# Kernel tuning notes

Hardware: AMD Instinct MI355X
Metric: run time of the kernel (lower is better)

## Reference

```python
import jax, jax.numpy as jnp
import numpy as np

N = 100000      # nodes
E = 3200000     # edges (avg degree 32)
F_IN = 128      # num_node_features
H = 16          # hidden dim (fixed in module)
C = 2           # num_classes


def setup_inputs() -> dict:
    key = jax.random.key(0)
    k0, k1, k2, k3 = jax.random.split(key, 4)
    x = jax.random.normal(k0, (N, F_IN), dtype=jnp.float32)
    edge_index = jax.random.randint(k1, (2, E), 0, N, dtype=jnp.int32)
    # GCNConv params: weight (in,out) + bias (out,) per layer (glorot-ish scale)
    W1 = jax.random.normal(k2, (F_IN, H), dtype=jnp.float32) * (1.0 / np.sqrt(F_IN))
    b1 = jnp.zeros((H,), jnp.float32)
    W2 = jax.random.normal(k3, (H, C), dtype=jnp.float32) * (1.0 / np.sqrt(H))
    b2 = jnp.zeros((C,), jnp.float32)
    return {"x": x, "edge_index": edge_index, "W1": W1, "b1": b1, "W2": W2, "b2": b2}


def _gcn_conv(x, W, b, src, dst, n):
    # GCNConv: h = D^{-1/2}(A+I)D^{-1/2} (x W) + b, with self-loops in src/dst
    h = x @ W                                   # [n, out]
    deg = jax.ops.segment_sum(jnp.ones_like(dst, dtype=h.dtype), dst, num_segments=n)
    dinv = jnp.where(deg > 0, jax.lax.rsqrt(deg), 0.0)
    norm = dinv[src] * dinv[dst]                # [E+n]
    msg = h[src] * norm[:, None]                # gather + scale
    out = jax.ops.segment_sum(msg, dst, num_segments=n)  # scatter-add
    return out + b


def reference(x, edge_index, W1, b1, W2, b2):
    loops = jnp.arange(N, dtype=edge_index.dtype)
    src = jnp.concatenate([edge_index[0], loops])
    dst = jnp.concatenate([edge_index[1], loops])
    h = jax.nn.relu(_gcn_conv(x, W1, b1, src, dst, N))
    # F.dropout(training=False) in eval mode is identity
    out = _gcn_conv(h, W2, b2, src, dst, N)
    return jax.nn.log_softmax(out, axis=1)
```

## Files before the change

### kernel.cpp

```cpp
#include <hip/hip_runtime.h>
#include <hip/hip_bf16.h>

#define NN 100000
#define NE 3200000
#define FIN 128
#define HD 16
#define CD 2

#define BSH 8
#define BSPAN 256
#define NBKT 391
#define CAP 9216
#define NPB 391

#define FXS 1048576.0f
#define FXI (1.0f / 1048576.0f)

__device__ __forceinline__ float lo2f(unsigned int u) {
    union { float f; unsigned int i; } v; v.i = u << 16; return v.f;
}
__device__ __forceinline__ float hi2f(unsigned int u) {
    union { float f; unsigned int i; } v; v.i = u & 0xFFFF0000u; return v.f;
}
__device__ __forceinline__ ushort f2b(float f) {
    union { float f; unsigned int u; } v; v.f = f;
    unsigned int r = (v.u + 0x7FFFu + ((v.u >> 16) & 1u)) >> 16;
    return (ushort)r;
}
__device__ __forceinline__ unsigned pck(float a, float b) {
    return (unsigned)f2b(a) | ((unsigned)f2b(b) << 16);
}

__global__ __launch_bounds__(512) void k_scat(const int* __restrict__ src,
                                              const int* __restrict__ dst,
                                              int* __restrict__ gcnt,
                                              unsigned int* __restrict__ csrb) {
    __shared__ int h[NBKT];
    __shared__ int cur[NBKT];
    int t = threadIdx.x;
    for (int i = t; i < NBKT; i += 512) h[i] = 0;
    __syncthreads();
    int cq = blockIdx.x * 2048;
    const int4* s4p = (const int4*)src;
    const int4* d4p = (const int4*)dst;
    int4 sv[4], dv[4];
    #pragma unroll
    for (int j = 0; j < 4; ++j) {
        int e4 = cq + j * 512 + t;
        if (e4 < NE / 4) {
            sv[j] = s4p[e4];
            dv[j] = d4p[e4];
            atomicAdd(&h[dv[j].x >> BSH], 1);
            atomicAdd(&h[dv[j].y >> BSH], 1);
            atomicAdd(&h[dv[j].z >> BSH], 1);
            atomicAdd(&h[dv[j].w >> BSH], 1);
        }
    }
    __syncthreads();
    for (int i = t; i < NBKT; i += 512) {
        int c = h[i];
        int base = c ? atomicAdd(&gcnt[i], c) : 0;
        cur[i] = i * CAP + base;
    }
    __syncthreads();
    #pragma unroll
    for (int j = 0; j < 4; ++j) {
        int e4 = cq + j * 512 + t;
        if (e4 < NE / 4) {
            int p;
            p = atomicAdd(&cur[dv[j].x >> BSH], 1);
            csrb[p] = (unsigned)sv[j].x | ((unsigned)(dv[j].x & (BSPAN - 1)) << 17);
            p = atomicAdd(&cur[dv[j].y >> BSH], 1);
            csrb[p] = (unsigned)sv[j].y | ((unsigned)(dv[j].y & (BSPAN - 1)) << 17);
            p = atomicAdd(&cur[dv[j].z >> BSH], 1);
            csrb[p] = (unsigned)sv[j].z | ((unsigned)(dv[j].z & (BSPAN - 1)) << 17);
            p = atomicAdd(&cur[dv[j].w >> BSH], 1);
            csrb[p] = (unsigned)sv[j].w | ((unsigned)(dv[j].w & (BSPAN - 1)) << 17);
        }
    }
}

__global__ __launch_bounds__(512) void k_gemm1d(const int* __restrict__ gcnt,
                                                const unsigned int* __restrict__ csrb,
                                                const float* __restrict__ x,
                                                const float* __restrict__ W1,
                                                float* __restrict__ dinv,
                                                ushort* __restrict__ h1b) {
    __shared__ float wsm[FIN][HD];
    __shared__ int cnt[BSPAN];
    __shared__ float dvs[BSPAN];
    int b = blockIdx.x, t = threadIdx.x;
    if (t < BSPAN) cnt[t] = 0;
    for (int i = t; i < FIN * HD; i += 512) wsm[i >> 4][i & 15] = W1[i];
    __syncthreads();
    int e0 = b * CAP, e1 = e0 + gcnt[b];
    for (int e = e0 + t; e < e1; e += 512) atomicAdd(&cnt[csrb[e] >> 17], 1);
    __syncthreads();
    if (t < BSPAN) {
        int node = b * BSPAN + t;
        float di = rsqrtf((float)cnt[t] + 1.0f);
        dvs[t] = di;
        if (node < NN) dinv[node] = di;
    }
    __syncthreads();
    int loc = t >> 1, half = t & 1;
    int node = b * BSPAN + loc;
    if (node >= NN) return;
    int g = half * 8;
    const float4* xr = (const float4*)(x + (size_t)node * FIN);
    float a0 = 0.f, a1 = 0.f, a2 = 0.f, a3 = 0.f;
    float a4 = 0.f, a5 = 0.f, a6 = 0.f, a7 = 0.f;
    #pragma unroll
    for (int k4 = 0; k4 < FIN / 4; ++k4) {
        float4 v = xr[k4];
        #pragma unroll
        for (int kk = 0; kk < 4; ++kk) {
            float vk = (kk == 0) ? v.x : (kk == 1) ? v.y : (kk == 2) ? v.z : v.w;
            float4 w0 = *(const float4*)&wsm[k4 * 4 + kk][g];
            float4 w1 = *(const float4*)&wsm[k4 * 4 + kk][g + 4];
            a0 += vk * w0.x; a1 += vk * w0.y; a2 += vk * w0.z; a3 += vk * w0.w;
            a4 += vk * w1.x; a5 += vk * w1.y; a6 += vk * w1.z; a7 += vk * w1.w;
        }
    }
    float di = dvs[loc];
    uint4 r = {pck(a0 * di, a1 * di), pck(a2 * di, a3 * di),
               pck(a4 * di, a5 * di), pck(a6 * di, a7 * di)};
    *(uint4*)(h1b + (size_t)node * HD + g) = r;
}

__device__ __forceinline__ void scat16(int* a, uint4 u0, uint4 u1) {
    atomicAdd(a + 0,  __float2int_rn(lo2f(u0.x) * FXS));
    atomicAdd(a + 1,  __float2int_rn(hi2f(u0.x) * FXS));
    atomicAdd(a + 2,  __float2int_rn(lo2f(u0.y) * FXS));
    atomicAdd(a + 3,  __float2int_rn(hi2f(u0.y) * FXS));
    atomicAdd(a + 4,  __float2int_rn(lo2f(u0.z) * FXS));
    atomicAdd(a + 5,  __float2int_rn(hi2f(u0.z) * FXS));
    atomicAdd(a + 6,  __float2int_rn(lo2f(u0.w) * FXS));
    atomicAdd(a + 7,  __float2int_rn(hi2f(u0.w) * FXS));
    atomicAdd(a + 8,  __float2int_rn(lo2f(u1.x) * FXS));
    atomicAdd(a + 9,  __float2int_rn(hi2f(u1.x) * FXS));
    atomicAdd(a + 10, __float2int_rn(lo2f(u1.y) * FXS));
    atomicAdd(a + 11, __float2int_rn(hi2f(u1.y) * FXS));
    atomicAdd(a + 12, __float2int_rn(lo2f(u1.z) * FXS));
    atomicAdd(a + 13, __float2int_rn(hi2f(u1.z) * FXS));
    atomicAdd(a + 14, __float2int_rn(lo2f(u1.w) * FXS));
    atomicAdd(a + 15, __float2int_rn(hi2f(u1.w) * FXS));
}

__global__ __launch_bounds__(512) void k_aggs1(const int* __restrict__ gcnt,
                                               const unsigned int* __restrict__ csrb,
                                               const ushort* __restrict__ h1b,
                                               const float* __restrict__ dinv,
                                               const float* __restrict__ b1,
                                               const float* __restrict__ W2,
                                               float* __restrict__ g_s) {
    __shared__ int acc[BSPAN][HD + 1];
    __shared__ float w2s[HD * 2];
    __shared__ float b1s[HD];
    int b = blockIdx.x, t = threadIdx.x;
    for (int i = t; i < BSPAN * (HD + 1); i += 512) ((int*)acc)[i] = 0;
    if (t < HD * 2) w2s[t] = W2[t];
    else if (t < HD * 3) b1s[t - HD * 2] = b1[t - HD * 2];
    __syncthreads();
    int e0 = b * CAP, e1 = e0 + gcnt[b];
    int e = e0 + t;
    for (; e + 512 < e1; e += 1024) {
        unsigned pa = csrb[e];
        unsigned pb = csrb[e + 512];
        const uint4* ra = (const uint4*)(h1b + (size_t)(pa & 0x1FFFF) * HD);
        const uint4* rb = (const uint4*)(h1b + (size_t)(pb & 0x1FFFF) * HD);
        uint4 a0 = ra[0], a1 = ra[1];
        uint4 c0 = rb[0], c1 = rb[1];
        scat16(acc[pa >> 17], a0, a1);
        scat16(acc[pb >> 17], c0, c1);
    }
    if (e < e1) {
        unsigned p = csrb[e];
        const uint4* r = (const uint4*)(h1b + (size_t)(p & 0x1FFFF) * HD);
        uint4 u0 = r[0], u1 = r[1];
        scat16(acc[p >> 17], u0, u1);
    }
    __syncthreads();
    int loc = t >> 1, half = t & 1;
    int node = b * BSPAN + loc;
    if (node < NN) {
        float di = dinv[node];
        const uint4 sv = *(const uint4*)(h1b + (size_t)node * HD + half * 8);
        float sf[8] = {lo2f(sv.x), hi2f(sv.x), lo2f(sv.y), hi2f(sv.y),
                       lo2f(sv.z), hi2f(sv.z), lo2f(sv.w), hi2f(sv.w)};
        const int* a = acc[loc] + half * 8;
        const float* bb = b1s + half * 8;
        const float* ww = w2s + half * 16;
        float p0 = 0.f, p1 = 0.f;
        #pragma unroll
        for (int k = 0; k < 8; ++k) {
            float v = fmaxf(di * ((float)a[k] * FXI + sf[k]) + bb[k], 0.f);
            p0 += v * ww[k * 2];
            p1 += v * ww[k * 2 + 1];
        }
        p0 += __shfl_xor(p0, 1, 64);
        p1 += __shfl_xor(p1, 1, 64);
        if (half == 0) {
            float2 r = {p0 * di, p1 * di};
            *(float2*)(g_s + (size_t)node * 2) = r;
        }
    }
}

__global__ __launch_bounds__(512) void k_aggs2(const int* __restrict__ gcnt,
                                               const unsigned int* __restrict__ csrb,
                                               const float* __restrict__ g_s,
                                               const float* __restrict__ dinv,
                                               const float* __restrict__ b2,
                                               float* __restrict__ out) {
    __shared__ int acc[BSPAN * 3];
    int b = blockIdx.x, t = threadIdx.x;
    for (int i = t; i < BSPAN * 3; i += 512) acc[i] = 0;
    __syncthreads();
    int e0 = b * CAP, e1 = e0 + gcnt[b];
    int e = e0 + t;
    for (; e + 512 < e1; e += 1024) {
        unsigned pa = csrb[e];
        unsigned pb = csrb[e + 512];
        float2 va = *(const float2*)(g_s + (size_t)(pa & 0x1FFFF) * 2);
        float2 vb = *(const float2*)(g_s + (size_t)(pb & 0x1FFFF) * 2);
        int la = (pa >> 17) * 3, lb = (pb >> 17) * 3;
        atomicAdd(&acc[la],     __float2int_rn(va.x * FXS));
        atomicAdd(&acc[la + 1], __float2int_rn(va.y * FXS));
        atomicAdd(&acc[lb],     __float2int_rn(vb.x * FXS));
        atomicAdd(&acc[lb + 1], __float2int_rn(vb.y * FXS));
    }
    if (e < e1) {
        unsigned p = csrb[e];
        float2 v = *(const float2*)(g_s + (size_t)(p & 0x1FFFF) * 2);
        int l = (p >> 17) * 3;
        atomicAdd(&acc[l],     __float2int_rn(v.x * FXS));
        atomicAdd(&acc[l + 1], __float2int_rn(v.y * FXS));
    }
    __syncthreads();
    if (t < BSPAN) {
        int node = b * BSPAN + t;
        if (node < NN) {
            float di = dinv[node];
            float2 sv = *(const float2*)(g_s + (size_t)node * 2);
            float o0 = di * ((float)acc[t * 3] * FXI + sv.x) + b2[0];
            float o1 = di * ((float)acc[t * 3 + 1] * FXI + sv.y) + b2[1];
            float mx = fmaxf(o0, o1);
            float l = mx + logf(__expf(o0 - mx) + __expf(o1 - mx));
            float2 r = {o0 - l, o1 - l};
            *(float2*)(out + (size_t)node * 2) = r;
        }
    }
}

extern "C" void kernel_launch(void* const* d_in, const int* in_sizes, int n_in,
                              void* d_out, int out_size, void* d_ws, size_t ws_size,
                              hipStream_t stream) {
    const float* x   = (const float*)d_in[0];
    const int* ei    = (const int*)d_in[1];
    const int* src   = ei;
    const int* dst   = ei + NE;
    const float* W1  = (const float*)d_in[2];
    const float* b1  = (const float*)d_in[3];
    const float* W2  = (const float*)d_in[4];
    const float* b2  = (const float*)d_in[5];
    float* out = (float*)d_out;

    char* w = (char*)d_ws;
    int*   gcnt        = (int*)w;            w += NBKT * 4;
    float* dinv        = (float*)w;          w += NN * 4;
    unsigned int* csrb = (unsigned int*)w;   w += (size_t)NBKT * CAP * 4;
    ushort* h1b        = (ushort*)w;         w += (size_t)NN * HD * 2;
    float* g_s         = (float*)w;          w += NN * CD * 4;

    hipMemsetAsync(gcnt, 0, NBKT * 4, stream);
    k_scat   <<<NPB, 512, 0, stream>>>(src, dst, gcnt, csrb);
    k_gemm1d <<<NBKT, 512, 0, stream>>>(gcnt, csrb, x, W1, dinv, h1b);
    k_aggs1  <<<NBKT, 512, 0, stream>>>(gcnt, csrb, h1b, dinv, b1, W2, g_s);
    k_aggs2  <<<NBKT, 512, 0, stream>>>(gcnt, csrb, g_s, dinv, b2, out);
}
```

Before: 200.6 us.

## Fuse all GCN stages into one persistent kernel with grid barriers

Merges the four kernels into a single persistent kernel of 391 blocks that synchronise through a software grid barrier built on global atomics, and keeps the per-node degree scaling in shared memory instead of a global dinv array. The bucket scatter now stages edges in LDS, prefix-sums the bucket counts, and writes contiguous runs to the global CSR buffer, which should make those writes better coalesced. This removes three launch boundaries, but it depends on every block being co-resident for the spin barrier to avoid deadlock, and the larger union of shared memory may lower occupancy.

```diff
diff --git a/kernel.cpp b/kernel.cpp
--- a/kernel.cpp
+++ b/kernel.cpp
@@ -1,131 +1,60 @@
 #include <hip/hip_runtime.h>
-#include <hip/hip_bf16.h>
 
 #define NN 100000
 #define NE 3200000
 #define FIN 128
 #define HD 16
-#define CD 2
 
 #define BSH 8
 #define BSPAN 256
 #define NBKT 391
 #define CAP 9216
-#define NPB 391
+#define TPB 512
 
 #define FXS 1048576.0f
 #define FXI (1.0f / 1048576.0f)
 
-__device__ __forceinline__ float lo2f(unsigned int u) {
-    union { float f; unsigned int i; } v; v.i = u << 16; return v.f;
-}
-__device__ __forceinline__ float hi2f(unsigned int u) {
-    union { float f; unsigned int i; } v; v.i = u & 0xFFFF0000u; return v.f;
+__device__ __forceinline__ float lo2f(unsigned u) {
+    union { float f; unsigned i; } v; v.i = u << 16; return v.f;
+}
+__device__ __forceinline__ float hi2f(unsigned u) {
+    union { float f; unsigned i; } v; v.i = u & 0xFFFF0000u; return v.f;
 }
 __device__ __forceinline__ ushort f2b(float f) {
-    union { float f; unsigned int u; } v; v.f = f;
-    unsigned int r = (v.u + 0x7FFFu + ((v.u >> 16) & 1u)) >> 16;
+    union { float f; unsigned u; } v; v.f = f;
+    unsigned r = (v.u + 0x7FFFu + ((v.u >> 16) & 1u)) >> 16;
     return (ushort)r;
 }
 __device__ __forceinline__ unsigned pck(float a, float b) {
     return (unsigned)f2b(a) | ((unsigned)f2b(b) << 16);
 }
 
-__global__ __launch_bounds__(512) void k_scat(const int* __restrict__ src,
-                                              const int* __restrict__ dst,
-                                              int* __restrict__ gcnt,
-                                              unsigned int* __restrict__ csrb) {
-    __shared__ int h[NBKT];
-    __shared__ int cur[NBKT];
-    int t = threadIdx.x;
-    for (int i = t; i < NBKT; i += 512) h[i] = 0;
-    __syncthreads();
-    int cq = blockIdx.x * 2048;
-    const int4* s4p = (const int4*)src;
-    const int4* d4p = (const int4*)dst;
-    int4 sv[4], dv[4];
-    #pragma unroll
-    for (int j = 0; j < 4; ++j) {
-        int e4 = cq + j * 512 + t;
-        if (e4 < NE / 4) {
-            sv[j] = s4p[e4];
-            dv[j] = d4p[e4];
-            atomicAdd(&h[dv[j].x >> BSH], 1);
-            atomicAdd(&h[dv[j].y >> BSH], 1);
-            atomicAdd(&h[dv[j].z >> BSH], 1);
-            atomicAdd(&h[dv[j].w >> BSH], 1);
-        }
-    }
-    __syncthreads();
-    for (int i = t; i < NBKT; i += 512) {
-        int c = h[i];
-        int base = c ? atomicAdd(&gcnt[i], c) : 0;
-        cur[i] = i * CAP + base;
-    }
-    __syncthreads();
-    #pragma unroll
-    for (int j = 0; j < 4; ++j) {
-        int e4 = cq + j * 512 + t;
-        if (e4 < NE / 4) {
-            int p;
-            p = atomicAdd(&cur[dv[j].x >> BSH], 1);
-            csrb[p] = (unsigned)sv[j].x | ((unsigned)(dv[j].x & (BSPAN - 1)) << 17);
-            p = atomicAdd(&cur[dv[j].y >> BSH], 1);
-            csrb[p] = (unsigned)sv[j].y | ((unsigned)(dv[j].y & (BSPAN - 1)) << 17);
-            p = atomicAdd(&cur[dv[j].z >> BSH], 1);
-            csrb[p] = (unsigned)sv[j].z | ((unsigned)(dv[j].z & (BSPAN - 1)) << 17);
-            p = atomicAdd(&cur[dv[j].w >> BSH], 1);
-            csrb[p] = (unsigned)sv[j].w | ((unsigned)(dv[j].w & (BSPAN - 1)) << 17);
-        }
-    }
-}
-
-__global__ __launch_bounds__(512) void k_gemm1d(const int* __restrict__ gcnt,
-                                                const unsigned int* __restrict__ csrb,
-                                                const float* __restrict__ x,
-                                                const float* __restrict__ W1,
-                                                float* __restrict__ dinv,
-                                                ushort* __restrict__ h1b) {
-    __shared__ float wsm[FIN][HD];
-    __shared__ int cnt[BSPAN];
-    __shared__ float dvs[BSPAN];
-    int b = blockIdx.x, t = threadIdx.x;
-    if (t < BSPAN) cnt[t] = 0;
-    for (int i = t; i < FIN * HD; i += 512) wsm[i >> 4][i & 15] = W1[i];
-    __syncthreads();
-    int e0 = b * CAP, e1 = e0 + gcnt[b];
-    for (int e = e0 + t; e < e1; e += 512) atomicAdd(&cnt[csrb[e] >> 17], 1);
-    __syncthreads();
-    if (t < BSPAN) {
-        int node = b * BSPAN + t;
-        float di = rsqrtf((float)cnt[t] + 1.0f);
-        dvs[t] = di;
-        if (node < NN) dinv[node] = di;
-    }
-    __syncthreads();
-    int loc = t >> 1, half = t & 1;
-    int node = b * BSPAN + loc;
-    if (node >= NN) return;
-    int g = half * 8;
-    const float4* xr = (const float4*)(x + (size_t)node * FIN);
-    float a0 = 0.f, a1 = 0.f, a2 = 0.f, a3 = 0.f;
-    float a4 = 0.f, a5 = 0.f, a6 = 0.f, a7 = 0.f;
-    #pragma unroll
-    for (int k4 = 0; k4 < FIN / 4; ++k4) {
-        float4 v = xr[k4];
-        #pragma unroll
-        for (int kk = 0; kk < 4; ++kk) {
-            float vk = (kk == 0) ? v.x : (kk == 1) ? v.y : (kk == 2) ? v.z : v.w;
-            float4 w0 = *(const float4*)&wsm[k4 * 4 + kk][g];
-            float4 w1 = *(const float4*)&wsm[k4 * 4 + kk][g + 4];
-            a0 += vk * w0.x; a1 += vk * w0.y; a2 += vk * w0.z; a3 += vk * w0.w;
-            a4 += vk * w1.x; a5 += vk * w1.y; a6 += vk * w1.z; a7 += vk * w1.w;
-        }
-    }
-    float di = dvs[loc];
-    uint4 r = {pck(a0 * di, a1 * di), pck(a2 * di, a3 * di),
-               pck(a4 * di, a5 * di), pck(a6 * di, a7 * di)};
-    *(uint4*)(h1b + (size_t)node * HD + g) = r;
+union SMem {
+    struct { int h[NBKT]; int sbuf[TPB]; int lcur[NBKT]; int gbase[NBKT];
+             unsigned ebuf[8192]; } s;
+    struct { float wsm[FIN][HD]; int cnt[BSPAN]; } g;
+    struct { int acc[BSPAN][HD + 1]; float w2s[HD * 2]; float b1s[HD]; } a1;
+    struct { int acc2[BSPAN * 3]; } a2;
+};
+
+__device__ __forceinline__ void gbar(int* bar, int phase) {
+    __syncthreads();
+    if (threadIdx.x == 0) {
+        __threadfence();
+        __hip_atomic_fetch_add(&bar[0], 1, __ATOMIC_RELEASE, __HIP_MEMORY_SCOPE_AGENT);
+        if (blockIdx.x == 0) {
+            while (__hip_atomic_load(&bar[0], __ATOMIC_ACQUIRE, __HIP_MEMORY_SCOPE_AGENT)
+                   < phase * NBKT)
+                __builtin_amdgcn_s_sleep(4);
+            __hip_atomic_store(&bar[1], phase, __ATOMIC_RELEASE, __HIP_MEMORY_SCOPE_AGENT);
+        } else {
+            while (__hip_atomic_load(&bar[1], __ATOMIC_ACQUIRE, __HIP_MEMORY_SCOPE_AGENT)
+                   < phase)
+                __builtin_amdgcn_s_sleep(4);
+        }
+        __threadfence();
+    }
+    __syncthreads();
 }
 
 __device__ __forceinline__ void scat16(int* a, uint4 u0, uint4 u1) {
@@ -147,104 +76,200 @@
     atomicAdd(a + 15, __float2int_rn(hi2f(u1.w) * FXS));
 }
 
-__global__ __launch_bounds__(512) void k_aggs1(const int* __restrict__ gcnt,
-                                               const unsigned int* __restrict__ csrb,
-                                               const ushort* __restrict__ h1b,
-                                               const float* __restrict__ dinv,
-                                               const float* __restrict__ b1,
-                                               const float* __restrict__ W2,
-                                               float* __restrict__ g_s) {
-    __shared__ int acc[BSPAN][HD + 1];
-    __shared__ float w2s[HD * 2];
-    __shared__ float b1s[HD];
+__global__ __launch_bounds__(TPB, 4) void k_all(
+    const int* __restrict__ src, const int* __restrict__ dst,
+    const float* __restrict__ x, const float* __restrict__ W1,
+    const float* __restrict__ b1, const float* __restrict__ W2,
+    const float* __restrict__ b2,
+    int* __restrict__ gcnt, int* __restrict__ bar,
+    unsigned* __restrict__ csrb, ushort* __restrict__ h1b,
+    float* __restrict__ g_s, float* __restrict__ out)
+{
+    __shared__ SMem sm;
+    __shared__ float dvs[BSPAN];
     int b = blockIdx.x, t = threadIdx.x;
-    for (int i = t; i < BSPAN * (HD + 1); i += 512) ((int*)acc)[i] = 0;
-    if (t < HD * 2) w2s[t] = W2[t];
-    else if (t < HD * 3) b1s[t - HD * 2] = b1[t - HD * 2];
-    __syncthreads();
+
+    for (int i = t; i < NBKT; i += TPB) sm.s.h[i] = 0;
+    __syncthreads();
+    int cq = b * 2048;
+    const int4* s4p = (const int4*)src;
+    const int4* d4p = (const int4*)dst;
+    int4 sv[4], dv[4];
+    #pragma unroll
+    for (int j = 0; j < 4; ++j) {
+        int e4 = cq + j * TPB + t;
+        if (e4 < NE / 4) {
+            sv[j] = s4p[e4]; dv[j] = d4p[e4];
+            atomicAdd(&sm.s.h[dv[j].x >> BSH], 1);
+            atomicAdd(&sm.s.h[dv[j].y >> BSH], 1);
+            atomicAdd(&sm.s.h[dv[j].z >> BSH], 1);
+            atomicAdd(&sm.s.h[dv[j].w >> BSH], 1);
+        }
+    }
+    __syncthreads();
+    sm.s.sbuf[t] = (t < NBKT) ? sm.s.h[t] : 0;
+    __syncthreads();
+    for (int off = 1; off < TPB; off <<= 1) {
+        int v = 0;
+        if (t >= off) v = sm.s.sbuf[t - off];
+        __syncthreads();
+        if (t >= off) sm.s.sbuf[t] += v;
+        __syncthreads();
+    }
+    if (t < NBKT) {
+        int c = sm.s.h[t];
+        int excl = sm.s.sbuf[t] - c;
+        sm.s.lcur[t] = excl;
+        int gb = t * CAP - excl;
+        if (c) gb += atomicAdd(&gcnt[t], c);
+        sm.s.gbase[t] = gb;
+    }
+    __syncthreads();
+    #pragma unroll
+    for (int j = 0; j < 4; ++j) {
+        int e4 = cq + j * TPB + t;
+        if (e4 < NE / 4) {
+            int bk, p;
+            bk = dv[j].x >> BSH; p = atomicAdd(&sm.s.lcur[bk], 1);
+            sm.s.ebuf[p] = (unsigned)sv[j].x | ((unsigned)(dv[j].x & (BSPAN - 1)) << 17);
+            bk = dv[j].y >> BSH; p = atomicAdd(&sm.s.lcur[bk], 1);
+            sm.s.ebuf[p] = (unsigned)sv[j].y | ((unsigned)(dv[j].y & (BSPAN - 1)) << 17);
+            bk = dv[j].z >> BSH; p = atomicAdd(&sm.s.lcur[bk], 1);
+            sm.s.ebuf[p] = (unsigned)sv[j].z | ((unsigned)(dv[j].z & (BSPAN - 1)) << 17);
+            bk = dv[j].w >> BSH; p = atomicAdd(&sm.s.lcur[bk], 1);
+            sm.s.ebuf[p] = (unsigned)sv[j].w | ((unsigned)(dv[j].w & (BSPAN - 1)) << 17);
+        }
+    }
+    __syncthreads();
+    int ecnt = NE - b * 8192; if (ecnt > 8192) ecnt = 8192;
+    for (int p = t; p < ecnt; p += TPB) {
+        unsigned pl = sm.s.ebuf[p];
+        int lo = 0, hi = NBKT;
+        while (lo < hi) { int mid = (lo + hi) >> 1;
+                          if (sm.s.sbuf[mid] > p) hi = mid; else lo = mid + 1; }
+        csrb[sm.s.gbase[lo] + p] = pl;
+    }
+    gbar(bar, 1);
+
     int e0 = b * CAP, e1 = e0 + gcnt[b];
-    int e = e0 + t;
-    for (; e + 512 < e1; e += 1024) {
-        unsigned pa = csrb[e];
-        unsigned pb = csrb[e + 512];
-        const uint4* ra = (const uint4*)(h1b + (size_t)(pa & 0x1FFFF) * HD);
-        const uint4* rb = (const uint4*)(h1b + (size_t)(pb & 0x1FFFF) * HD);
-        uint4 a0 = ra[0], a1 = ra[1];
-        uint4 c0 = rb[0], c1 = rb[1];
-        scat16(acc[pa >> 17], a0, a1);
-        scat16(acc[pb >> 17], c0, c1);
-    }
-    if (e < e1) {
-        unsigned p = csrb[e];
-        const uint4* r = (const uint4*)(h1b + (size_t)(p & 0x1FFFF) * HD);
-        uint4 u0 = r[0], u1 = r[1];
-        scat16(acc[p >> 17], u0, u1);
-    }
-    __syncthreads();
-    int loc = t >> 1, half = t & 1;
-    int node = b * BSPAN + loc;
-    if (node < NN) {
-        float di = dinv[node];
-        const uint4 sv = *(const uint4*)(h1b + (size_t)node * HD + half * 8);
-        float sf[8] = {lo2f(sv.x), hi2f(sv.x), lo2f(sv.y), hi2f(sv.y),
-                       lo2f(sv.z), hi2f(sv.z), lo2f(sv.w), hi2f(sv.w)};
-        const int* a = acc[loc] + half * 8;
-        const float* bb = b1s + half * 8;
-        const float* ww = w2s + half * 16;
-        float p0 = 0.f, p1 = 0.f;
-        #pragma unroll
-        for (int k = 0; k < 8; ++k) {
-            float v = fmaxf(di * ((float)a[k] * FXI + sf[k]) + bb[k], 0.f);
-            p0 += v * ww[k * 2];
-            p1 += v * ww[k * 2 + 1];
-        }
-        p0 += __shfl_xor(p0, 1, 64);
-        p1 += __shfl_xor(p1, 1, 64);
-        if (half == 0) {
-            float2 r = {p0 * di, p1 * di};
-            *(float2*)(g_s + (size_t)node * 2) = r;
-        }
-    }
-}
-
-__global__ __launch_bounds__(512) void k_aggs2(const int* __restrict__ gcnt,
-                                               const unsigned int* __restrict__ csrb,
-                                               const float* __restrict__ g_s,
-                                               const float* __restrict__ dinv,
-                                               const float* __restrict__ b2,
-                                               float* __restrict__ out) {
-    __shared__ int acc[BSPAN * 3];
-    int b = blockIdx.x, t = threadIdx.x;
-    for (int i = t; i < BSPAN * 3; i += 512) acc[i] = 0;
-    __syncthreads();
-    int e0 = b * CAP, e1 = e0 + gcnt[b];
-    int e = e0 + t;
-    for (; e + 512 < e1; e += 1024) {
-        unsigned pa = csrb[e];
-        unsigned pb = csrb[e + 512];
-        float2 va = *(const float2*)(g_s + (size_t)(pa & 0x1FFFF) * 2);
-        float2 vb = *(const float2*)(g_s + (size_t)(pb & 0x1FFFF) * 2);
-        int la = (pa >> 17) * 3, lb = (pb >> 17) * 3;
-        atomicAdd(&acc[la],     __float2int_rn(va.x * FXS));
-        atomicAdd(&acc[la + 1], __float2int_rn(va.y * FXS));
-        atomicAdd(&acc[lb],     __float2int_rn(vb.x * FXS));
-        atomicAdd(&acc[lb + 1], __float2int_rn(vb.y * FXS));
-    }
-    if (e < e1) {
-        unsigned p = csrb[e];
-        float2 v = *(const float2*)(g_s + (size_t)(p & 0x1FFFF) * 2);
-        int l = (p >> 17) * 3;
-        atomicAdd(&acc[l],     __float2int_rn(v.x * FXS));
-        atomicAdd(&acc[l + 1], __float2int_rn(v.y * FXS));
+    for (int i = t; i < FIN * HD; i += TPB) sm.g.wsm[i >> 4][i & 15] = W1[i];
+    if (t < BSPAN) sm.g.cnt[t] = 0;
+    __syncthreads();
+    for (int e = e0 + t; e < e1; e += TPB) atomicAdd(&sm.g.cnt[csrb[e] >> 17], 1);
+    __syncthreads();
+    if (t < BSPAN) dvs[t] = rsqrtf((float)sm.g.cnt[t] + 1.0f);
+    __syncthreads();
+    {
+        int loc = t >> 1, half = t & 1;
+        int node = b * BSPAN + loc;
+        if (node < NN) {
+            int g8 = half * 8;
+            const float4* xr = (const float4*)(x + (size_t)node * FIN);
+            float a0 = 0.f, a1 = 0.f, a2 = 0.f, a3 = 0.f;
+            float a4 = 0.f, a5 = 0.f, a6 = 0.f, a7 = 0.f;
+            #pragma unroll
+            for (int k4 = 0; k4 < FIN / 4; ++k4) {
+                float4 v = xr[k4];
+                #pragma unroll
+                for (int kk = 0; kk < 4; ++kk) {
+                    float vk = (kk == 0) ? v.x : (kk == 1) ? v.y : (kk == 2) ? v.z : v.w;
+                    float4 w0 = *(const float4*)&sm.g.wsm[k4 * 4 + kk][g8];
+                    float4 w1 = *(const float4*)&sm.g.wsm[k4 * 4 + kk][g8 + 4];
+                    a0 += vk * w0.x; a1 += vk * w0.y; a2 += vk * w0.z; a3 += vk * w0.w;
+                    a4 += vk * w1.x; a5 += vk * w1.y; a6 += vk * w1.z; a7 += vk * w1.w;
+                }
+            }
+            float di = dvs[loc];
+            uint4 r = {pck(a0 * di, a1 * di), pck(a2 * di, a3 * di),
+                       pck(a4 * di, a5 * di), pck(a6 * di, a7 * di)};
+            *(uint4*)(h1b + (size_t)node * HD + g8) = r;
+        }
+    }
+    gbar(bar, 2);
+
+    for (int i = t; i < BSPAN * (HD + 1); i += TPB) ((int*)sm.a1.acc)[i] = 0;
+    if (t < HD * 2) sm.a1.w2s[t] = W2[t];
+    else if (t < HD * 3) sm.a1.b1s[t - HD * 2] = b1[t - HD * 2];
+    __syncthreads();
+    {
+        int e = e0 + t;
+        for (; e + TPB < e1; e += 2 * TPB) {
+            unsigned pa = csrb[e];
+            unsigned pb = csrb[e + TPB];
+            const uint4* ra = (const uint4*)(h1b + (size_t)(pa & 0x1FFFF) * HD);
+            const uint4* rb = (const uint4*)(h1b + (size_t)(pb & 0x1FFFF) * HD);
+            uint4 a0 = ra[0], a1 = ra[1];
+            uint4 c0 = rb[0], c1 = rb[1];
+            scat16(sm.a1.acc[pa >> 17], a0, a1);
+            scat16(sm.a1.acc[pb >> 17], c0, c1);
+        }
+        if (e < e1) {
+            unsigned p = csrb[e];
+            const uint4* r = (const uint4*)(h1b + (size_t)(p & 0x1FFFF) * HD);
+            uint4 u0 = r[0], u1 = r[1];
+            scat16(sm.a1.acc[p >> 17], u0, u1);
+        }
+    }
+    __syncthreads();
+    {
+        int loc = t >> 1, half = t & 1;
+        int node = b * BSPAN + loc;
+        if (node < NN) {
+            float di = dvs[loc];
+            const uint4 svv = *(const uint4*)(h1b + (size_t)node * HD + half * 8);
+            float sf[8] = {lo2f(svv.x), hi2f(svv.x), lo2f(svv.y), hi2f(svv.y),
+                           lo2f(svv.z), hi2f(svv.z), lo2f(svv.w), hi2f(svv.w)};
+            const int* a = sm.a1.acc[loc] + half * 8;
+            const float* bb = sm.a1.b1s + half * 8;
+            const float* ww = sm.a1.w2s + half * 16;
+            float p0 = 0.f, p1 = 0.f;
+            #pragma unroll
+            for (int k = 0; k < 8; ++k) {
+                float v = fmaxf(di * ((float)a[k] * FXI + sf[k]) + bb[k], 0.f);
+                p0 += v * ww[k * 2];
+                p1 += v * ww[k * 2 + 1];
+            }
+            p0 += __shfl_xor(p0, 1, 64);
+            p1 += __shfl_xor(p1, 1, 64);
+            if (half == 0) {
+                float2 r = {p0 * di, p1 * di};
+                *(float2*)(g_s + (size_t)node * 2) = r;
+            }
+        }
+    }
+    gbar(bar, 3);
+
+    for (int i = t; i < BSPAN * 3; i += TPB) sm.a2.acc2[i] = 0;
+    __syncthreads();
+    {
+        int e = e0 + t;
+        for (; e + TPB < e1; e += 2 * TPB) {
+            unsigned pa = csrb[e];
+            unsigned pb = csrb[e + TPB];
+            float2 va = *(const float2*)(g_s + (size_t)(pa & 0x1FFFF) * 2);
+            float2 vb = *(const float2*)(g_s + (size_t)(pb & 0x1FFFF) * 2);
+            int la = (pa >> 17) * 3, lb = (pb >> 17) * 3;
+            atomicAdd(&sm.a2.acc2[la],     __float2int_rn(va.x * FXS));
+            atomicAdd(&sm.a2.acc2[la + 1], __float2int_rn(va.y * FXS));
+            atomicAdd(&sm.a2.acc2[lb],     __float2int_rn(vb.x * FXS));
+            atomicAdd(&sm.a2.acc2[lb + 1], __float2int_rn(vb.y * FXS));
+        }
+        if (e < e1) {
+            unsigned p = csrb[e];
+            float2 v = *(const float2*)(g_s + (size_t)(p & 0x1FFFF) * 2);
+            int l = (p >> 17) * 3;
+            atomicAdd(&sm.a2.acc2[l],     __float2int_rn(v.x * FXS));
+            atomicAdd(&sm.a2.acc2[l + 1], __float2int_rn(v.y * FXS));
+        }
     }
     __syncthreads();
     if (t < BSPAN) {
         int node = b * BSPAN + t;
         if (node < NN) {
-            float di = dinv[node];
-            float2 sv = *(const float2*)(g_s + (size_t)node * 2);
-            float o0 = di * ((float)acc[t * 3] * FXI + sv.x) + b2[0];
-            float o1 = di * ((float)acc[t * 3 + 1] * FXI + sv.y) + b2[1];
+            float di = dvs[t];
+            float2 svv = *(const float2*)(g_s + (size_t)node * 2);
+            float o0 = di * ((float)sm.a2.acc2[t * 3] * FXI + svv.x) + b2[0];
+            float o1 = di * ((float)sm.a2.acc2[t * 3 + 1] * FXI + svv.y) + b2[1];
             float mx = fmaxf(o0, o1);
             float l = mx + logf(__expf(o0 - mx) + __expf(o1 - mx));
             float2 r = {o0 - l, o1 - l};
@@ -268,14 +293,12 @@
 
     char* w = (char*)d_ws;
     int*   gcnt        = (int*)w;            w += NBKT * 4;
-    float* dinv        = (float*)w;          w += NN * 4;
+    int*   bar         = (int*)w;            w += 2 * 4;
     unsigned int* csrb = (unsigned int*)w;   w += (size_t)NBKT * CAP * 4;
     ushort* h1b        = (ushort*)w;         w += (size_t)NN * HD * 2;
-    float* g_s         = (float*)w;          w += NN * CD * 4;
-
-    hipMemsetAsync(gcnt, 0, NBKT * 4, stream);
-    k_scat   <<<NPB, 512, 0, stream>>>(src, dst, gcnt, csrb);
-    k_gemm1d <<<NBKT, 512, 0, stream>>>(gcnt, csrb, x, W1, dinv, h1b);
-    k_aggs1  <<<NBKT, 512, 0, stream>>>(gcnt, csrb, h1b, dinv, b1, W2, g_s);
-    k_aggs2  <<<NBKT, 512, 0, stream>>>(gcnt, csrb, g_s, dinv, b2, out);
-}
+    float* g_s         = (float*)w;          w += NN * 2 * 4;
+
+    hipMemsetAsync(gcnt, 0, (NBKT + 2) * 4, stream);
+    k_all<<<NBKT, TPB, 0, stream>>>(src, dst, x, W1, b1, W2, b2,
+                                    gcnt, bar, csrb, h1b, g_s, out);
+}
```

Measured after the change: 504.5 us. +151.5%, slower.

## Stage edge scatter in shared memory sorted by bucket before global writes

Applied to the files above, without the earlier changes.

The bucketing kernel now computes a block-local prefix sum over bucket counts and places each edge into a shared-memory buffer ordered by bucket. It then writes the buffer to global memory in linear order, finding each entry's bucket by binary search, so consecutive threads write contiguous runs instead of scattering single words. This is meant to cut uncoalesced global stores in the CSR build. The cost is about 32KB of extra shared memory per block, which may lower occupancy, plus a scan and a per-element binary search.

```diff
diff --git a/kernel.cpp b/kernel.cpp
--- a/kernel.cpp
+++ b/kernel.cpp
@@ -1,55 +1,55 @@
 #include <hip/hip_runtime.h>
-#include <hip/hip_bf16.h>
 
 #define NN 100000
 #define NE 3200000
 #define FIN 128
 #define HD 16
-#define CD 2
 
 #define BSH 8
 #define BSPAN 256
 #define NBKT 391
 #define CAP 9216
-#define NPB 391
+#define TPB 512
 
 #define FXS 1048576.0f
 #define FXI (1.0f / 1048576.0f)
 
-__device__ __forceinline__ float lo2f(unsigned int u) {
-    union { float f; unsigned int i; } v; v.i = u << 16; return v.f;
-}
-__device__ __forceinline__ float hi2f(unsigned int u) {
-    union { float f; unsigned int i; } v; v.i = u & 0xFFFF0000u; return v.f;
+__device__ __forceinline__ float lo2f(unsigned u) {
+    union { float f; unsigned i; } v; v.i = u << 16; return v.f;
+}
+__device__ __forceinline__ float hi2f(unsigned u) {
+    union { float f; unsigned i; } v; v.i = u & 0xFFFF0000u; return v.f;
 }
 __device__ __forceinline__ ushort f2b(float f) {
-    union { float f; unsigned int u; } v; v.f = f;
-    unsigned int r = (v.u + 0x7FFFu + ((v.u >> 16) & 1u)) >> 16;
+    union { float f; unsigned u; } v; v.f = f;
+    unsigned r = (v.u + 0x7FFFu + ((v.u >> 16) & 1u)) >> 16;
     return (ushort)r;
 }
 __device__ __forceinline__ unsigned pck(float a, float b) {
     return (unsigned)f2b(a) | ((unsigned)f2b(b) << 16);
 }
 
-__global__ __launch_bounds__(512) void k_scat(const int* __restrict__ src,
+__global__ __launch_bounds__(TPB) void k_scat(const int* __restrict__ src,
                                               const int* __restrict__ dst,
                                               int* __restrict__ gcnt,
-                                              unsigned int* __restrict__ csrb) {
+                                              unsigned* __restrict__ csrb) {
     __shared__ int h[NBKT];
-    __shared__ int cur[NBKT];
-    int t = threadIdx.x;
-    for (int i = t; i < NBKT; i += 512) h[i] = 0;
-    __syncthreads();
-    int cq = blockIdx.x * 2048;
+    __shared__ int sbuf[TPB];
+    __shared__ int lcur[NBKT];
+    __shared__ int gbase[NBKT];
+    __shared__ unsigned ebuf[8192];
+    int b = blockIdx.x, t = threadIdx.x;
+    for (int i = t; i < NBKT; i += TPB) h[i] = 0;
+    __syncthreads();
+    int cq = b * 2048;
     const int4* s4p = (const int4*)src;
     const int4* d4p = (const int4*)dst;
     int4 sv[4], dv[4];
     #pragma unroll
     for (int j = 0; j < 4; ++j) {
-        int e4 = cq + j * 512 + t;
+        int e4 = cq + j * TPB + t;
         if (e4 < NE / 4) {
-            sv[j] = s4p[e4];
-            dv[j] = d4p[e4];
+            sv[j] = s4p[e4]; dv[j] = d4p[e4];
             atomicAdd(&h[dv[j].x >> BSH], 1);
             atomicAdd(&h[dv[j].y >> BSH], 1);
             atomicAdd(&h[dv[j].z >> BSH], 1);
@@ -57,30 +57,51 @@
         }
     }
     __syncthreads();
-    for (int i = t; i < NBKT; i += 512) {
-        int c = h[i];
-        int base = c ? atomicAdd(&gcnt[i], c) : 0;
-        cur[i] = i * CAP + base;
+    sbuf[t] = (t < NBKT) ? h[t] : 0;
+    __syncthreads();
+    for (int off = 1; off < TPB; off <<= 1) {
+        int v = 0;
+        if (t >= off) v = sbuf[t - off];
+        __syncthreads();
+        if (t >= off) sbuf[t] += v;
+        __syncthreads();
+    }
+    if (t < NBKT) {
+        int c = h[t];
+        int excl = sbuf[t] - c;
+        lcur[t] = excl;
+        int gb = t * CAP - excl;
+        if (c) gb += atomicAdd(&gcnt[t], c);
+        gbase[t] = gb;
     }
     __syncthreads();
     #pragma unroll
     for (int j = 0; j < 4; ++j) {
-        int e4 = cq + j * 512 + t;
+        int e4 = cq + j * TPB + t;
         if (e4 < NE / 4) {
-            int p;
-            p = atomicAdd(&cur[dv[j].x >> BSH], 1);
-            csrb[p] = (unsigned)sv[j].x | ((unsigned)(dv[j].x & (BSPAN - 1)) << 17);
-            p = atomicAdd(&cur[dv[j].y >> BSH], 1);
-            csrb[p] = (unsigned)sv[j].y | ((unsigned)(dv[j].y & (BSPAN - 1)) << 17);
-            p = atomicAdd(&cur[dv[j].z >> BSH], 1);
-            csrb[p] = (unsigned)sv[j].z | ((unsigned)(dv[j].z & (BSPAN - 1)) << 17);
-            p = atomicAdd(&cur[dv[j].w >> BSH], 1);
-            csrb[p] = (unsigned)sv[j].w | ((unsigned)(dv[j].w & (BSPAN - 1)) << 17);
-        }
-    }
-}
-
-__global__ __launch_bounds__(512) void k_gemm1d(const int* __restrict__ gcnt,
+            int bk, p;
+            bk = dv[j].x >> BSH; p = atomicAdd(&lcur[bk], 1);
+            ebuf[p] = (unsigned)sv[j].x | ((unsigned)(dv[j].x & (BSPAN - 1)) << 17);
+            bk = dv[j].y >> BSH; p = atomicAdd(&lcur[bk], 1);
+            ebuf[p] = (unsigned)sv[j].y | ((unsigned)(dv[j].y & (BSPAN - 1)) << 17);
+            bk = dv[j].z >> BSH; p = atomicAdd(&lcur[bk], 1);
+            ebuf[p] = (unsigned)sv[j].z | ((unsigned)(dv[j].z & (BSPAN - 1)) << 17);
+            bk = dv[j].w >> BSH; p = atomicAdd(&lcur[bk], 1);
+            ebuf[p] = (unsigned)sv[j].w | ((unsigned)(dv[j].w & (BSPAN - 1)) << 17);
+        }
+    }
+    __syncthreads();
+    int ecnt = NE - b * 8192; if (ecnt > 8192) ecnt = 8192;
+    for (int p = t; p < ecnt; p += TPB) {
+        unsigned pl = ebuf[p];
+        int lo = 0, hi = NBKT;
+        while (lo < hi) { int mid = (lo + hi) >> 1;
+                          if (sbuf[mid] > p) hi = mid; else lo = mid + 1; }
+        csrb[gbase[lo] + p] = pl;
+    }
+}
+
+__global__ __launch_bounds__(TPB) void k_gemm1d(const int* __restrict__ gcnt,
                                                 const unsigned int* __restrict__ csrb,
                                                 const float* __restrict__ x,
                                                 const float* __restrict__ W1,
@@ -91,10 +112,10 @@
     __shared__ float dvs[BSPAN];
     int b = blockIdx.x, t = threadIdx.x;
     if (t < BSPAN) cnt[t] = 0;
-    for (int i = t; i < FIN * HD; i += 512) wsm[i >> 4][i & 15] = W1[i];
+    for (int i = t; i < FIN * HD; i += TPB) wsm[i >> 4][i & 15] = W1[i];
     __syncthreads();
     int e0 = b * CAP, e1 = e0 + gcnt[b];
-    for (int e = e0 + t; e < e1; e += 512) atomicAdd(&cnt[csrb[e] >> 17], 1);
+    for (int e = e0 + t; e < e1; e += TPB) atomicAdd(&cnt[csrb[e] >> 17], 1);
     __syncthreads();
     if (t < BSPAN) {
         int node = b * BSPAN + t;
@@ -147,7 +168,7 @@
     atomicAdd(a + 15, __float2int_rn(hi2f(u1.w) * FXS));
 }
 
-__global__ __launch_bounds__(512) void k_aggs1(const int* __restrict__ gcnt,
+__global__ __launch_bounds__(TPB) void k_aggs1(const int* __restrict__ gcnt,
                                                const unsigned int* __restrict__ csrb,
                                                const ushort* __restrict__ h1b,
                                                const float* __restrict__ dinv,
@@ -158,15 +179,15 @@
     __shared__ float w2s[HD * 2];
     __shared__ float b1s[HD];
     int b = blockIdx.x, t = threadIdx.x;
-    for (int i = t; i < BSPAN * (HD + 1); i += 512) ((int*)acc)[i] = 0;
+    for (int i = t; i < BSPAN * (HD + 1); i += TPB) ((int*)acc)[i] = 0;
     if (t < HD * 2) w2s[t] = W2[t];
     else if (t < HD * 3) b1s[t - HD * 2] = b1[t - HD * 2];
     __syncthreads();
     int e0 = b * CAP, e1 = e0 + gcnt[b];
     int e = e0 + t;
-    for (; e + 512 < e1; e += 1024) {
+    for (; e + TPB < e1; e += 2 * TPB) {
         unsigned pa = csrb[e];
-        unsigned pb = csrb[e + 512];
+        unsigned pb = csrb[e + TPB];
         const uint4* ra = (const uint4*)(h1b + (size_t)(pa & 0x1FFFF) * HD);
         const uint4* rb = (const uint4*)(h1b + (size_t)(pb & 0x1FFFF) * HD);
         uint4 a0 = ra[0], a1 = ra[1];
@@ -207,7 +228,7 @@
     }
 }
 
-__global__ __launch_bounds__(512) void k_aggs2(const int* __restrict__ gcnt,
+__global__ __launch_bounds__(TPB) void k_aggs2(const int* __restrict__ gcnt,
                                                const unsigned int* __restrict__ csrb,
                                                const float* __restrict__ g_s,
                                                const float* __restrict__ dinv,
@@ -215,13 +236,13 @@
                                                float* __restrict__ out) {
     __shared__ int acc[BSPAN * 3];
     int b = blockIdx.x, t = threadIdx.x;
-    for (int i = t; i < BSPAN * 3; i += 512) acc[i] = 0;
+    for (int i = t; i < BSPAN * 3; i += TPB) acc[i] = 0;
     __syncthreads();
     int e0 = b * CAP, e1 = e0 + gcnt[b];
     int e = e0 + t;
-    for (; e + 512 < e1; e += 1024) {
+    for (; e + TPB < e1; e += 2 * TPB) {
         unsigned pa = csrb[e];
-        unsigned pb = csrb[e + 512];
+        unsigned pb = csrb[e + TPB];
         float2 va = *(const float2*)(g_s + (size_t)(pa & 0x1FFFF) * 2);
         float2 vb = *(const float2*)(g_s + (size_t)(pb & 0x1FFFF) * 2);
         int la = (pa >> 17) * 3, lb = (pb >> 17) * 3;
@@ -271,11 +292,11 @@
     float* dinv        = (float*)w;          w += NN * 4;
     unsigned int* csrb = (unsigned int*)w;   w += (size_t)NBKT * CAP * 4;
     ushort* h1b        = (ushort*)w;         w += (size_t)NN * HD * 2;
-    float* g_s         = (float*)w;          w += NN * CD * 4;
+    float* g_s         = (float*)w;          w += NN * 2 * 4;
 
     hipMemsetAsync(gcnt, 0, NBKT * 4, stream);
-    k_scat   <<<NPB, 512, 0, stream>>>(src, dst, gcnt, csrb);
-    k_gemm1d <<<NBKT, 512, 0, stream>>>(gcnt, csrb, x, W1, dinv, h1b);
-    k_aggs1  <<<NBKT, 512, 0, stream>>>(gcnt, csrb, h1b, dinv, b1, W2, g_s);
-    k_aggs2  <<<NBKT, 512, 0, stream>>>(gcnt, csrb, g_s, dinv, b2, out);
-}
+    k_scat   <<<NBKT, TPB, 0, stream>>>(src, dst, gcnt, csrb);
+    k_gemm1d <<<NBKT, TPB, 0, stream>>>(gcnt, csrb, x, W1, dinv, h1b);
+    k_aggs1  <<<NBKT, TPB, 0, stream>>>(gcnt, csrb, h1b, dinv, b1, W2, g_s);
+    k_aggs2  <<<NBKT, TPB, 0, stream>>>(gcnt, csrb, g_s, dinv, b2, out);
+}
```

New measurement: 200.2 us, median of 2. About the same (-0.2%).
